# Optimization experiments

Measured on AMD Instinct MI355X. Metric: run time of the kernel, lower is better.

## Reference

```python
import jax, jax.numpy as jnp
import numpy as np

N_STREAMS = 4
N_HEADS = 4
D_STATE = 64
EPS_RMS = float(np.finfo(np.float32).eps)


def rms_norm(x, w):
    v = jnp.mean(x * x, axis=-1, keepdims=True)
    return x * jax.lax.rsqrt(v + EPS_RMS) * w


def sinkhorn_mix(logits, iters=5):
    n = logits.shape[0]
    M = jax.nn.sigmoid(logits) + jnp.eye(n, dtype=logits.dtype)
    for _ in range(iters):
        M = M / (M.sum(axis=1, keepdims=True) + 1e-6)
        M = M / (M.sum(axis=0, keepdims=True) + 1e-6)
    return M


def mamba_block(u, norm_w, Wi, bi, A_log, D, dt_bias, Wo, bo):
    B, L, d_model = u.shape
    d_in = 2 * d_model
    P = d_in // N_HEADS
    un = rms_norm(u, norm_w)
    zxbcdt = un @ Wi + bi  # [B,L,4612]
    z = zxbcdt[:, :, :d_in]
    x = zxbcdt[:, :, d_in:2 * d_in].reshape(B, L, N_HEADS, P)
    dt = zxbcdt[:, :, 2 * d_in:2 * d_in + N_HEADS]
    BC = zxbcdt[:, :, 2 * d_in + N_HEADS:].reshape(B, L, N_HEADS, 2, D_STATE)
    B_mat, C_mat = BC[:, :, :, 0], BC[:, :, :, 1]
    dt = jax.nn.softplus(dt + dt_bias)            # [B,L,H]
    A = -jnp.exp(A_log)                            # [H]
    dtA = jnp.exp(dt * A)                          # [B,L,H]
    dtB = dt[..., None] * B_mat                    # [B,L,H,N]

    # time-major scan over the selective-state recurrence
    def step(h, inp):
        dtA_t, dtB_t, x_t, C_t = inp               # [B,H],[B,H,N],[B,H,P],[B,H,N]
        h = h * dtA_t[:, :, None, None] + dtB_t[..., None] * x_t[:, :, None, :]
        y_t = jnp.einsum('bhn,bhnp->bhp', C_t, h)
        return h, y_t

    h0 = jnp.zeros((B, N_HEADS, D_STATE, P), dtype=u.dtype)
    xs = (jnp.moveaxis(dtA, 1, 0), jnp.moveaxis(dtB, 1, 0),
          jnp.moveaxis(x, 1, 0), jnp.moveaxis(C_mat, 1, 0))
    _, ys = jax.lax.scan(step, h0, xs)             # ys: [L,B,H,P]
    y = jnp.moveaxis(ys, 0, 1)                     # [B,L,H,P]
    y = y + x * D[None, None, :, None]
    y = y.reshape(B, L, d_in) * jax.nn.silu(z)
    return y @ Wo + bo


def setup_inputs() -> dict:
    key = jax.random.key(0)
    ks = jax.random.split(key, 10)
    B, L, d_model, vocab, n_layers = 2, 2048, 1024, 32000, 4
    d_proj_out = 2 * 2 * d_model + 2 * N_HEADS * D_STATE + N_HEADS  # 4612
    d_in = 2 * d_model
    s = lambda f: 1.0 / np.sqrt(f)
    return {
        'tokens': jax.random.randint(ks[0], (B, L), 0, vocab, dtype=jnp.int32),
        'embed': jax.random.normal(ks[1], (vocab, d_model), jnp.float32) * 0.02,
        'norm_w': jnp.ones((n_layers, d_model), jnp.float32),
        'in_proj_W': jax.random.normal(ks[2], (n_layers, d_model, d_proj_out), jnp.float32) * s(d_model),
        'in_proj_b': jnp.zeros((n_layers, d_proj_out), jnp.float32),
        'A_log': jnp.full((n_layers, N_HEADS), -4.0, jnp.float32),
        'D': jnp.ones((n_layers, N_HEADS), jnp.float32),
        'dt_bias': jax.random.uniform(ks[3], (n_layers, N_HEADS), jnp.float32) - 4.0,
        'out_proj_W': jax.random.normal(ks[4], (n_layers, d_in, d_model), jnp.float32) * s(d_in),
        'out_proj_b': jnp.zeros((n_layers, d_model), jnp.float32),
        'mixer_logits': jax.random.normal(ks[5], (n_layers, N_STREAMS, N_STREAMS), jnp.float32) * 0.1,
        'norm_f_w': jnp.ones((d_model,), jnp.float32),
        'head_W': jax.random.normal(ks[6], (d_model, vocab), jnp.float32) * s(d_model),
        'head_b': jnp.zeros((vocab,), jnp.float32),
    }


def reference(tokens, embed, norm_w, in_proj_W, in_proj_b, A_log, D, dt_bias,
              out_proj_W, out_proj_b, mixer_logits, norm_f_w, head_W, head_b):
    B, L = tokens.shape
    d_model = embed.shape[1]
    d_sub = d_model // N_STREAMS
    x = embed[tokens]                              # [B,L,d_model]
    H = x.reshape(B, L, N_STREAMS, d_sub)
    n_layers = norm_w.shape[0]
    for l in range(n_layers):
        M = sinkhorn_mix(mixer_logits[l])
        H_res = jnp.einsum('bsid,ji->bsjd', H, M)
        x_out = mamba_block(H.reshape(B, L, d_model), norm_w[l], in_proj_W[l],
                            in_proj_b[l], A_log[l], D[l], dt_bias[l],
                            out_proj_W[l], out_proj_b[l])
        H = H_res + x_out.reshape(B, L, N_STREAMS, d_sub)
    out = rms_norm(H.reshape(B, L, d_model), norm_f_w)
    return out @ head_W + head_b
```

## Files before the change

kernel.cpp:

```cpp
#include <hip/hip_runtime.h>
#include <hip/hip_fp16.h>
#include <cstdint>


typedef _Float16 f16;
typedef __attribute__((ext_vector_type(8))) _Float16 f16x8;
typedef __attribute__((ext_vector_type(4))) _Float16 f16x4;
typedef __attribute__((ext_vector_type(4))) float f32x4;

#define LDS_CAST(p) ((__attribute__((address_space(3))) void*)(p))
#define GLB_CAST(p) ((const __attribute__((address_space(1))) void*)(p))

static __device__ __forceinline__ void gload16(const void* g, void* l) {
    __builtin_amdgcn_global_load_lds(GLB_CAST(g), LDS_CAST(l), 16, 0, 0);
}

__global__ __launch_bounds__(256) void gemm_f16(
    const f16* __restrict__ A, const f16* __restrict__ Bt,
    const float* __restrict__ bias, float* __restrict__ C,
    int M, int N, int K)
{
    __shared__ f16 As[128 * 32];
    __shared__ f16 Bs[128 * 32];
    const int t = threadIdx.x;
    const int lane = t & 63;
    const int w = t >> 6;
    const int m0 = blockIdx.y * 128, n0 = blockIdx.x * 128;
    const int wm0 = (w >> 1) * 64, wn0 = (w & 1) * 64;
    const int mrow = lane & 15, ksel = lane >> 4;

    f32x4 zero = {0.f, 0.f, 0.f, 0.f};
    f32x4 acc[4][4];
#pragma unroll
    for (int i = 0; i < 4; i++)
#pragma unroll
        for (int j = 0; j < 4; j++) acc[i][j] = zero;

    const f16* Abase = A + (size_t)m0 * K;
    const f16* Bbase = Bt + (size_t)n0 * K;

    for (int k0 = 0; k0 < K; k0 += 32) {
#pragma unroll
        for (int i = 0; i < 2; i++) {
            int lin = t + i * 256;
            int r = lin >> 2;
            int cc = (lin & 3) * 8;
            gload16(Abase + (size_t)r * K + k0 + cc, As + lin * 8);
            gload16(Bbase + (size_t)r * K + k0 + cc, Bs + lin * 8);
        }
        __syncthreads();
        f16x8 af[4], bf[4];
#pragma unroll
        for (int i = 0; i < 4; i++) {
            af[i] = *(const f16x8*)(As + (wm0 + i * 16 + mrow) * 32 + ksel * 8);
            bf[i] = *(const f16x8*)(Bs + (wn0 + i * 16 + mrow) * 32 + ksel * 8);
        }
#pragma unroll
        for (int i = 0; i < 4; i++)
#pragma unroll
            for (int j = 0; j < 4; j++)
                acc[i][j] = __builtin_amdgcn_mfma_f32_16x16x32_f16(af[i], bf[j], acc[i][j], 0, 0, 0);
        __syncthreads();
    }

    const int r0 = ksel * 4;
#pragma unroll
    for (int j = 0; j < 4; j++) {
        int col = n0 + wn0 + j * 16 + mrow;
        if (col < N) {
            float bv = bias ? bias[col] : 0.f;
#pragma unroll
            for (int i = 0; i < 4; i++) {
                int rowm = m0 + wm0 + i * 16 + r0;
#pragma unroll
                for (int r = 0; r < 4; r++)
                    C[(size_t)(rowm + r) * N + col] = acc[i][j][r] + bv;
            }
        }
    }
}

__global__ __launch_bounds__(256) void transpose_w(
    const float* __restrict__ W, f16* __restrict__ Wt, int K, int N, int Npad)
{
    __shared__ float tile[32][33];
    int n0 = blockIdx.x * 32, k0 = blockIdx.y * 32;
    int tx = threadIdx.x & 31, ty = threadIdx.x >> 5;
#pragma unroll
    for (int i = 0; i < 4; i++) {
        int k = k0 + ty + 8 * i;
        int n = n0 + tx;
        tile[ty + 8 * i][tx] = (n < N) ? W[(size_t)k * N + n] : 0.f;
    }
    __syncthreads();
#pragma unroll
    for (int i = 0; i < 4; i++) {
        int n = n0 + ty + 8 * i;
        if (n < Npad) Wt[(size_t)n * K + k0 + tx] = (f16)tile[tx][ty + 8 * i];
    }
}

__global__ void sinkhorn_k(const float* __restrict__ logits, float* __restrict__ Mout)
{
    if (threadIdx.x != 0 || blockIdx.x != 0) return;
    for (int l = 0; l < 4; l++) {
        float M[16];
        for (int i = 0; i < 16; i++) {
            float v = logits[l * 16 + i];
            M[i] = 1.f / (1.f + __expf(-v)) + ((i % 5) == 0 ? 1.f : 0.f);
        }
        for (int it = 0; it < 5; it++) {
            for (int r = 0; r < 4; r++) {
                float s = M[r*4] + M[r*4+1] + M[r*4+2] + M[r*4+3] + 1e-6f;
                for (int c = 0; c < 4; c++) M[r*4+c] /= s;
            }
            for (int c = 0; c < 4; c++) {
                float s = M[c] + M[4+c] + M[8+c] + M[12+c] + 1e-6f;
                for (int r = 0; r < 4; r++) M[r*4+c] /= s;
            }
        }
        for (int i = 0; i < 16; i++) Mout[l * 16 + i] = M[i];
    }
}

__global__ __launch_bounds__(256) void embed_gather(
    const int* __restrict__ tokens, const float* __restrict__ embed, float* __restrict__ H)
{
    int i = blockIdx.x * 256 + threadIdx.x;
    int tok = i >> 8, d4 = i & 255;
    int tk = tokens[tok];
    float4 v = ((const float4*)(embed + (size_t)tk * 1024))[d4];
    ((float4*)(H + (size_t)tok * 1024))[d4] = v;
}

__global__ __launch_bounds__(256) void rmsnorm_k(
    const float* __restrict__ X, const float* __restrict__ w, f16* __restrict__ out)
{
    int tok = blockIdx.x;
    int t = threadIdx.x;
    const float4 v = ((const float4*)(X + (size_t)tok * 1024))[t];
    float ss = v.x*v.x + v.y*v.y + v.z*v.z + v.w*v.w;
#pragma unroll
    for (int off = 32; off > 0; off >>= 1) ss += __shfl_down(ss, off, 64);
    __shared__ float wsum[4];
    if ((t & 63) == 0) wsum[t >> 6] = ss;
    __syncthreads();
    float tot = wsum[0] + wsum[1] + wsum[2] + wsum[3];
    float sc = rsqrtf(tot * (1.f / 1024.f) + 1.1920929e-07f);
    const float4 wv = ((const float4*)w)[t];
    f16x4 o;
    o[0] = (f16)(v.x * sc * wv.x);
    o[1] = (f16)(v.y * sc * wv.y);
    o[2] = (f16)(v.z * sc * wv.z);
    o[3] = (f16)(v.w * sc * wv.w);
    ((f16x4*)(out + (size_t)tok * 1024))[t] = o;
}

__global__ __launch_bounds__(256) void dt_cumsum(
    const float* __restrict__ zx, const float* __restrict__ dt_bias,
    const float* __restrict__ A_log,
    float* __restrict__ dt, float* __restrict__ cum, float* __restrict__ E)
{
    int bh = blockIdx.x;
    int b = bh >> 2, h = bh & 3;
    int t = threadIdx.x;
    float Ah = -__expf(A_log[h]);
    float bias = dt_bias[h];
    float run = 0.f, vals[8];
    for (int i = 0; i < 8; i++) {
        int l = t * 8 + i;
        float raw = zx[((size_t)(b * 2048 + l)) * 4612 + 4096 + h] + bias;
        float dtv = (raw > 20.f) ? raw : log1pf(__expf(raw));
        dt[bh * 2048 + l] = dtv;
        run += dtv * Ah;
        vals[i] = run;
    }
    __shared__ float ps[256];
    ps[t] = run;
    __syncthreads();
    for (int off = 1; off < 256; off <<= 1) {
        float v = (t >= off) ? ps[t - off] : 0.f;
        __syncthreads();
        ps[t] += v;
        __syncthreads();
    }
    float offset = (t > 0) ? ps[t - 1] : 0.f;
    for (int i = 0; i < 8; i++) {
        int l = t * 8 + i;
        float cv = vals[i] + offset;
        cum[bh * 2048 + l] = cv;
        if ((l & 63) == 63) E[bh * 32 + (l >> 6)] = cv;
    }
}

__global__ __launch_bounds__(256) void make_xT(
    const float* __restrict__ zx, f16* __restrict__ xT)
{
    int lb = blockIdx.x * 64, pb = blockIdx.y * 64, bh = blockIdx.z;
    int b = bh >> 2, h = bh & 3;
    __shared__ float tile[64][65];
    int tx = threadIdx.x & 63, ty = threadIdx.x >> 6;
#pragma unroll
    for (int i = 0; i < 16; i++) {
        int ll = ty + 4 * i;
        tile[ll][tx] = zx[((size_t)(b * 2048 + lb + ll)) * 4612 + 2048 + h * 512 + pb + tx];
    }
    __syncthreads();
#pragma unroll
    for (int i = 0; i < 16; i++) {
        int pl = ty + 4 * i;
        xT[((size_t)bh * 512 + pb + pl) * 2048 + lb + tx] = (f16)tile[tx][pl];
    }
}

__global__ __launch_bounds__(256) void make_BC(
    const float* __restrict__ zx, f16* __restrict__ Bc, f16* __restrict__ Cc)
{
    int i = blockIdx.x * 256 + threadIdx.x;
    int n = i & 63, h = (i >> 6) & 3, l = (i >> 8) & 2047, b = i >> 19;
    size_t rowoff = ((size_t)(b * 2048 + l)) * 4612 + 4100 + h * 128;
    size_t o = (((size_t)(b * 4 + h)) * 2048 + l) * 64 + n;
    Bc[o] = (f16)zx[rowoff + n];
    Cc[o] = (f16)zx[rowoff + 64 + n];
}

__global__ __launch_bounds__(256) void chunk_intra(
    const f16* __restrict__ Bc, const f16* __restrict__ Cc,
    const f16* __restrict__ xT,
    const float* __restrict__ dt, const float* __restrict__ cum,
    float* __restrict__ Y, float* __restrict__ Hloc)
{
    int c = blockIdx.x, bh = blockIdx.y;
    int l0 = c * 64;
    __shared__ f16 Cs[4096], Bs2[4096], Sb[4096], Wb[4096];
    __shared__ float cums[64], dts[64];
    int t = threadIdx.x;
    {
        const f16x8* sC = (const f16x8*)(Cc + ((size_t)bh * 2048 + l0) * 64);
        const f16x8* sB = (const f16x8*)(Bc + ((size_t)bh * 2048 + l0) * 64);
        ((f16x8*)Cs)[t] = sC[t];
        ((f16x8*)Cs)[t + 256] = sC[t + 256];
        ((f16x8*)Bs2)[t] = sB[t];
        ((f16x8*)Bs2)[t + 256] = sB[t + 256];
    }
    if (t < 64) {
        cums[t] = cum[bh * 2048 + l0 + t];
        dts[t] = dt[bh * 2048 + l0 + t];
    }
    __syncthreads();
    float cumEnd = cums[63];
#pragma unroll
    for (int q = 0; q < 16; q++) {
        int idx = t * 16 + q;
        int tt = idx >> 6, ss = idx & 63;
        float dot = 0.f;
        for (int n = 0; n < 64; n++)
            dot += (float)Cs[tt * 64 + n] * (float)Bs2[ss * 64 + n];
        float sv = (ss <= tt) ? dot * __expf(cums[tt] - cums[ss]) * dts[ss] : 0.f;
        Sb[idx] = (f16)sv;
        float wv = (float)Bs2[ss * 64 + tt] * __expf(cumEnd - cums[ss]) * dts[ss];
        Wb[tt * 64 + ss] = (f16)wv;
    }
    __syncthreads();

    int lane = t & 63, w = t >> 6;
    int mrow = lane & 15, ksel = lane >> 4;
    f16x8 sfr[2][4], wfr[2][4];
#pragma unroll
    for (int ks = 0; ks < 2; ks++)
#pragma unroll
        for (int mt = 0; mt < 4; mt++) {
            sfr[ks][mt] = *(const f16x8*)(Sb + (mt * 16 + mrow) * 64 + ks * 32 + ksel * 8);
            wfr[ks][mt] = *(const f16x8*)(Wb + (mt * 16 + mrow) * 64 + ks * 32 + ksel * 8);
        }
    const f16* xbase = xT + ((size_t)bh * 512) * 2048 + c * 64;
    f32x4 zero = {0.f, 0.f, 0.f, 0.f};
#pragma unroll
    for (int ph = 0; ph < 2; ph++) {
        int pb = w * 128 + ph * 64;
        f32x4 aY[4][4], aH[4][4];
#pragma unroll
        for (int i = 0; i < 4; i++)
#pragma unroll
            for (int j = 0; j < 4; j++) { aY[i][j] = zero; aH[i][j] = zero; }
#pragma unroll
        for (int ks = 0; ks < 2; ks++) {
#pragma unroll
            for (int nt = 0; nt < 4; nt++) {
                int pp = pb + nt * 16 + mrow;
                f16x8 bfv = *(const f16x8*)(xbase + (size_t)pp * 2048 + ks * 32 + ksel * 8);
#pragma unroll
                for (int mt = 0; mt < 4; mt++) {
                    aY[mt][nt] = __builtin_amdgcn_mfma_f32_16x16x32_f16(sfr[ks][mt], bfv, aY[mt][nt], 0, 0, 0);
                    aH[mt][nt] = __builtin_amdgcn_mfma_f32_16x16x32_f16(wfr[ks][mt], bfv, aH[mt][nt], 0, 0, 0);
                }
            }
        }
        int r0 = ksel * 4;
#pragma unroll
        for (int mt = 0; mt < 4; mt++)
#pragma unroll
            for (int nt = 0; nt < 4; nt++) {
                int pp = pb + nt * 16 + mrow;
#pragma unroll
                for (int r = 0; r < 4; r++) {
                    int tt = mt * 16 + r0 + r;
                    Y[((size_t)bh * 2048 + l0 + tt) * 512 + pp] = aY[mt][nt][r];
                    Hloc[(((size_t)bh * 32 + c) * 64 + tt) * 512 + pp] = aH[mt][nt][r];
                }
            }
    }
}

__global__ __launch_bounds__(256) void chunk_scan(
    const float* __restrict__ Hloc, const float* __restrict__ E,
    f16* __restrict__ HpreT)
{
    int bh = blockIdx.y;
    int p = blockIdx.x * 64 + (threadIdx.x & 63);
    int nb = (threadIdx.x >> 6) * 16;
    float h[16];
#pragma unroll
    for (int j = 0; j < 16; j++) h[j] = 0.f;
    float Eprev = 0.f;
    for (int c = 0; c < 32; c++) {
        size_t ob = (((size_t)bh * 32 + c) * 512 + p) * 64 + nb;
        f16x8 v0, v1;
#pragma unroll
        for (int j = 0; j < 8; j++) { v0[j] = (f16)h[j]; v1[j] = (f16)h[j + 8]; }
        *(f16x8*)(HpreT + ob) = v0;
        *(f16x8*)(HpreT + ob + 8) = v1;
        float Ec = E[bh * 32 + c];
        float decay = __expf(Ec - Eprev);
        Eprev = Ec;
        size_t ib = (((size_t)bh * 32 + c) * 64 + nb) * 512 + p;
#pragma unroll
        for (int j = 0; j < 16; j++)
            h[j] = decay * h[j] + Hloc[ib + (size_t)j * 512];
    }
}

__global__ __launch_bounds__(256) void chunk_inter(
    const f16* __restrict__ Cc, const f16* __restrict__ HpreT,
    const float* __restrict__ cum, const float* __restrict__ E,
    const float* __restrict__ Y, const float* __restrict__ zx,
    const float* __restrict__ Dp, f16* __restrict__ ybuf)
{
    int c = blockIdx.x, bh = blockIdx.y;
    int b = bh >> 2, h = bh & 3;
    int l0 = c * 64;
    __shared__ f16 Chat[4096];
    int t = threadIdx.x;
    float Eprev = (c > 0) ? E[bh * 32 + c - 1] : 0.f;
    for (int i = t; i < 4096; i += 256) {
        int tt = i >> 6, n = i & 63;
        float cv = (float)Cc[((size_t)bh * 2048 + l0 + tt) * 64 + n];
        Chat[i] = (f16)(cv * __expf(cum[bh * 2048 + l0 + tt] - Eprev));
    }
    __syncthreads();
    int lane = t & 63, w = t >> 6;
    int mrow = lane & 15, ksel = lane >> 4;
    float Dh = Dp[h];
    f16x8 af[2][4];
#pragma unroll
    for (int ks = 0; ks < 2; ks++)
#pragma unroll
        for (int mt = 0; mt < 4; mt++)
            af[ks][mt] = *(const f16x8*)(Chat + (mt * 16 + mrow) * 64 + ks * 32 + ksel * 8);
    const f16* hb = HpreT + (((size_t)bh * 32 + c) * 512) * 64;
    f32x4 zero = {0.f, 0.f, 0.f, 0.f};
#pragma unroll
    for (int ph = 0; ph < 2; ph++) {
        int pb = w * 128 + ph * 64;
        f32x4 acc[4][4];
#pragma unroll
        for (int i = 0; i < 4; i++)
#pragma unroll
            for (int j = 0; j < 4; j++) acc[i][j] = zero;
#pragma unroll
        for (int ks = 0; ks < 2; ks++) {
#pragma unroll
            for (int nt = 0; nt < 4; nt++) {
                int pp = pb + nt * 16 + mrow;
                f16x8 bfv = *(const f16x8*)(hb + (size_t)pp * 64 + ks * 32 + ksel * 8);
#pragma unroll
                for (int mt = 0; mt < 4; mt++)
                    acc[mt][nt] = __builtin_amdgcn_mfma_f32_16x16x32_f16(af[ks][mt], bfv, acc[mt][nt], 0, 0, 0);
            }
        }
        int r0 = ksel * 4;
#pragma unroll
        for (int mt = 0; mt < 4; mt++)
#pragma unroll
            for (int nt = 0; nt < 4; nt++) {
                int pp = pb + nt * 16 + mrow;
#pragma unroll
                for (int r = 0; r < 4; r++) {
                    int tt = mt * 16 + r0 + r;
                    int l = l0 + tt;
                    size_t zrow = ((size_t)(b * 2048 + l)) * 4612;
                    float y = acc[mt][nt][r] + Y[((size_t)bh * 2048 + l) * 512 + pp];
                    float x = zx[zrow + 2048 + h * 512 + pp];
                    y += x * Dh;
                    float z = zx[zrow + h * 512 + pp];
                    float sig = 1.f / (1.f + __expf(-z));
                    ybuf[((size_t)(b * 2048 + l)) * 2048 + h * 512 + pp] = (f16)(y * z * sig);
                }
            }
    }
}

__global__ __launch_bounds__(256) void mix_add(
    const float* __restrict__ Hold, const float* __restrict__ xout,
    const float* __restrict__ Mm, float* __restrict__ Hnew)
{
    int i = blockIdx.x * 256 + threadIdx.x;
    int j = i & 255, tok = i >> 8;
    size_t rb = (size_t)tok * 1024;
    float h0 = Hold[rb + j], h1 = Hold[rb + 256 + j];
    float h2 = Hold[rb + 512 + j], h3 = Hold[rb + 768 + j];
#pragma unroll
    for (int s = 0; s < 4; s++) {
        float v = Mm[s*4+0]*h0 + Mm[s*4+1]*h1 + Mm[s*4+2]*h2 + Mm[s*4+3]*h3
                + xout[rb + s * 256 + j];
        Hnew[rb + s * 256 + j] = v;
    }
}

extern "C" void kernel_launch(void* const* d_in, const int* in_sizes, int n_in,
                              void* d_out, int out_size, void* d_ws, size_t ws_size,
                              hipStream_t stream)
{
    const int*   tokens     = (const int*)d_in[0];
    const float* embed      = (const float*)d_in[1];
    const float* norm_w     = (const float*)d_in[2];
    const float* in_proj_W  = (const float*)d_in[3];
    const float* in_proj_b  = (const float*)d_in[4];
    const float* A_log      = (const float*)d_in[5];
    const float* Dp         = (const float*)d_in[6];
    const float* dt_bias    = (const float*)d_in[7];
    const float* out_proj_W = (const float*)d_in[8];
    const float* out_proj_b = (const float*)d_in[9];
    const float* mixer_log  = (const float*)d_in[10];
    const float* norm_f_w   = (const float*)d_in[11];
    const float* head_W     = (const float*)d_in[12];
    const float* head_b     = (const float*)d_in[13];
    float* out = (float*)d_out;
    (void)in_sizes; (void)n_in; (void)out_size; (void)ws_size;

    char* base = (char*)d_ws;
    size_t off = 0;
    auto alloc = [&](size_t bytes) -> void* {
        void* r = (void*)(base + off);
        off = (off + bytes + 255) & ~(size_t)255;
        return r;
    };
    f16*   WinT   = (f16*)alloc(4ull * 4736 * 1024 * 2);
    f16*   WoutT  = (f16*)alloc(4ull * 1024 * 2048 * 2);
    f16*   WheadT = (f16*)alloc(32000ull * 1024 * 2);
    float* Mall   = (float*)alloc(64 * 4);
    float* H0     = (float*)alloc(4096ull * 1024 * 4);
    float* H1     = (float*)alloc(4096ull * 1024 * 4);
    f16*   un     = (f16*)alloc(4096ull * 1024 * 2);
    float* zx     = (float*)alloc(4096ull * 4612 * 4);
    float* dtb    = (float*)alloc(8ull * 2048 * 4);
    float* cumb   = (float*)alloc(8ull * 2048 * 4);
    float* Eb     = (float*)alloc(8ull * 32 * 4);
    f16*   xT     = (f16*)alloc(8ull * 512 * 2048 * 2);
    f16*   Bc     = (f16*)alloc(8ull * 2048 * 64 * 2);
    f16*   Cc     = (f16*)alloc(8ull * 2048 * 64 * 2);
    float* Yb     = (float*)alloc(8ull * 2048 * 512 * 4);
    float* Hloc   = (float*)alloc(8ull * 32 * 64 * 512 * 4);
    f16*   HpreT  = (f16*)alloc(8ull * 32 * 512 * 64 * 2);
    f16*   ybuf   = (f16*)alloc(4096ull * 2048 * 2);
    float* xout   = (float*)alloc(4096ull * 1024 * 4);

    for (int l = 0; l < 4; l++) {
        transpose_w<<<dim3(148, 32), 256, 0, stream>>>(
            in_proj_W + (size_t)l * 1024 * 4612, WinT + (size_t)l * 4736 * 1024,
            1024, 4612, 4736);
        transpose_w<<<dim3(32, 64), 256, 0, stream>>>(
            out_proj_W + (size_t)l * 2048 * 1024, WoutT + (size_t)l * 1024 * 2048,
            2048, 1024, 1024);
    }
    transpose_w<<<dim3(1000, 32), 256, 0, stream>>>(head_W, WheadT, 1024, 32000, 32000);
    sinkhorn_k<<<1, 64, 0, stream>>>(mixer_log, Mall);
    embed_gather<<<4096, 256, 0, stream>>>(tokens, embed, H0);

    float* Hc = H0;
    float* Hn = H1;
    for (int l = 0; l < 4; l++) {
        rmsnorm_k<<<4096, 256, 0, stream>>>(Hc, norm_w + l * 1024, un);
        gemm_f16<<<dim3(37, 32), 256, 0, stream>>>(
            un, WinT + (size_t)l * 4736 * 1024, in_proj_b + l * 4612, zx,
            4096, 4612, 1024);
        dt_cumsum<<<8, 256, 0, stream>>>(zx, dt_bias + l * 4, A_log + l * 4, dtb, cumb, Eb);
        make_xT<<<dim3(32, 8, 8), 256, 0, stream>>>(zx, xT);
        make_BC<<<4096, 256, 0, stream>>>(zx, Bc, Cc);
        chunk_intra<<<dim3(32, 8), 256, 0, stream>>>(Bc, Cc, xT, dtb, cumb, Yb, Hloc);
        chunk_scan<<<dim3(8, 8), 256, 0, stream>>>(Hloc, Eb, HpreT);
        chunk_inter<<<dim3(32, 8), 256, 0, stream>>>(Cc, HpreT, cumb, Eb, Yb, zx, Dp + l * 4, ybuf);
        gemm_f16<<<dim3(8, 32), 256, 0, stream>>>(
            ybuf, WoutT + (size_t)l * 1024 * 2048, out_proj_b + l * 1024, xout,
            4096, 1024, 2048);
        mix_add<<<4096, 256, 0, stream>>>(Hc, xout, Mall + l * 16, Hn);
        float* tmp = Hc; Hc = Hn; Hn = tmp;
    }
    rmsnorm_k<<<4096, 256, 0, stream>>>(Hc, norm_f_w, un);
    gemm_f16<<<dim3(250, 32), 256, 0, stream>>>(un, WheadT, head_b, out, 4096, 32000, 1024);
}
```

Baseline: 2.273 ms.

## Swizzle GEMM tile order for XCD locality, vectorize epilogue, MFMA intra-chunk scores

The GEMM now remaps block IDs so consecutive work-groups on each XCD cover grouped M tiles. This improves L2 reuse of the weight and activation panels, and the grid dimensions are swapped to match. The MFMA operands are swapped so each lane holds four consecutive N columns, which allows float4 stores and bias loads in place of scalar strided stores. The chunk_intra C·B score computation moves from scalar per-thread dot products to MFMA. chunk_scan is split across a third grid dimension for more parallelism. The swizzle mapping treats the grid's x as the M-tile count, which relies on the launch dims being set consistently. The float4 accesses assume N is a multiple of four.

```diff
diff --git a/kernel.cpp b/kernel.cpp
--- a/kernel.cpp
+++ b/kernel.cpp
@@ -25,7 +25,24 @@
     const int t = threadIdx.x;
     const int lane = t & 63;
     const int w = t >> 6;
-    const int m0 = blockIdx.y * 128, n0 = blockIdx.x * 128;
+
+    const int gx = gridDim.x;
+    const int gy = gridDim.y;
+    const int nwg = gx * gy;
+    int lin = blockIdx.y * gx + blockIdx.x;
+    int xcd = lin & 7, loc = lin >> 3;
+    int q = nwg >> 3, rr = nwg & 7;
+    int wg = (xcd < rr) ? (xcd * (q + 1) + loc)
+                        : (rr * (q + 1) + (xcd - rr) * q + loc);
+    const int GROUP = 8;
+    int per_group = GROUP * gy;
+    int gid = wg / per_group;
+    int first_m = gid * GROUP;
+    int gsz = (gx - first_m < GROUP) ? (gx - first_m) : GROUP;
+    int inner = wg - gid * per_group;
+    const int m0 = (first_m + inner % gsz) * 128;
+    const int n0 = (inner / gsz) * 128;
+
     const int wm0 = (w >> 1) * 64, wn0 = (w & 1) * 64;
     const int mrow = lane & 15, ksel = lane >> 4;
 
@@ -42,11 +59,11 @@
     for (int k0 = 0; k0 < K; k0 += 32) {
 #pragma unroll
         for (int i = 0; i < 2; i++) {
-            int lin = t + i * 256;
-            int r = lin >> 2;
-            int cc = (lin & 3) * 8;
-            gload16(Abase + (size_t)r * K + k0 + cc, As + lin * 8);
-            gload16(Bbase + (size_t)r * K + k0 + cc, Bs + lin * 8);
+            int lin2 = t + i * 256;
+            int r = lin2 >> 2;
+            int cc = (lin2 & 3) * 8;
+            gload16(Abase + (size_t)r * K + k0 + cc, As + lin2 * 8);
+            gload16(Bbase + (size_t)r * K + k0 + cc, Bs + lin2 * 8);
         }
         __syncthreads();
         f16x8 af[4], bf[4];
@@ -59,22 +76,25 @@
         for (int i = 0; i < 4; i++)
 #pragma unroll
             for (int j = 0; j < 4; j++)
-                acc[i][j] = __builtin_amdgcn_mfma_f32_16x16x32_f16(af[i], bf[j], acc[i][j], 0, 0, 0);
+                acc[i][j] = __builtin_amdgcn_mfma_f32_16x16x32_f16(bf[j], af[i], acc[i][j], 0, 0, 0);
         __syncthreads();
     }
 
-    const int r0 = ksel * 4;
-#pragma unroll
-    for (int j = 0; j < 4; j++) {
-        int col = n0 + wn0 + j * 16 + mrow;
-        if (col < N) {
-            float bv = bias ? bias[col] : 0.f;
-#pragma unroll
-            for (int i = 0; i < 4; i++) {
-                int rowm = m0 + wm0 + i * 16 + r0;
-#pragma unroll
-                for (int r = 0; r < 4; r++)
-                    C[(size_t)(rowm + r) * N + col] = acc[i][j][r] + bv;
+#pragma unroll
+    for (int i = 0; i < 4; i++) {
+        int m = m0 + wm0 + i * 16 + mrow;
+#pragma unroll
+        for (int j = 0; j < 4; j++) {
+            int nb = n0 + wn0 + j * 16 + ksel * 4;
+            if (nb < N) {
+                float4 bv = {0.f, 0.f, 0.f, 0.f};
+                if (bias) bv = *(const float4*)(bias + nb);
+                float4 v;
+                v.x = acc[i][j][0] + bv.x;
+                v.y = acc[i][j][1] + bv.y;
+                v.z = acc[i][j][2] + bv.z;
+                v.w = acc[i][j][3] + bv.w;
+                *(float4*)(C + (size_t)m * N + nb) = v;
             }
         }
     }
@@ -249,22 +269,39 @@
     }
     __syncthreads();
     float cumEnd = cums[63];
-#pragma unroll
-    for (int q = 0; q < 16; q++) {
-        int idx = t * 16 + q;
-        int tt = idx >> 6, ss = idx & 63;
-        float dot = 0.f;
-        for (int n = 0; n < 64; n++)
-            dot += (float)Cs[tt * 64 + n] * (float)Bs2[ss * 64 + n];
-        float sv = (ss <= tt) ? dot * __expf(cums[tt] - cums[ss]) * dts[ss] : 0.f;
-        Sb[idx] = (f16)sv;
-        float wv = (float)Bs2[ss * 64 + tt] * __expf(cumEnd - cums[ss]) * dts[ss];
-        Wb[tt * 64 + ss] = (f16)wv;
-    }
-    __syncthreads();
-
     int lane = t & 63, w = t >> 6;
     int mrow = lane & 15, ksel = lane >> 4;
+
+    {
+        f16x8 cf[2];
+        cf[0] = *(const f16x8*)(Cs + (w * 16 + mrow) * 64 + ksel * 8);
+        cf[1] = *(const f16x8*)(Cs + (w * 16 + mrow) * 64 + 32 + ksel * 8);
+#pragma unroll
+        for (int j = 0; j < 4; j++) {
+            f32x4 d = {0.f, 0.f, 0.f, 0.f};
+#pragma unroll
+            for (int ks = 0; ks < 2; ks++) {
+                f16x8 bfv = *(const f16x8*)(Bs2 + (j * 16 + mrow) * 64 + ks * 32 + ksel * 8);
+                d = __builtin_amdgcn_mfma_f32_16x16x32_f16(cf[ks], bfv, d, 0, 0, 0);
+            }
+            int ss = j * 16 + mrow;
+#pragma unroll
+            for (int r = 0; r < 4; r++) {
+                int tt = w * 16 + ksel * 4 + r;
+                float sv = (ss <= tt) ? d[r] * __expf(cums[tt] - cums[ss]) * dts[ss] : 0.f;
+                Sb[tt * 64 + ss] = (f16)sv;
+            }
+        }
+#pragma unroll
+        for (int q2 = 0; q2 < 16; q2++) {
+            int idx = t * 16 + q2;
+            int tt = idx >> 6, ss = idx & 63;
+            float wv = (float)Bs2[ss * 64 + tt] * __expf(cumEnd - cums[ss]) * dts[ss];
+            Wb[tt * 64 + ss] = (f16)wv;
+        }
+    }
+    __syncthreads();
+
     f16x8 sfr[2][4], wfr[2][4];
 #pragma unroll
     for (int ks = 0; ks < 2; ks++)
@@ -318,24 +355,23 @@
 {
     int bh = blockIdx.y;
     int p = blockIdx.x * 64 + (threadIdx.x & 63);
-    int nb = (threadIdx.x >> 6) * 16;
-    float h[16];
-#pragma unroll
-    for (int j = 0; j < 16; j++) h[j] = 0.f;
+    int nb = blockIdx.z * 16 + (threadIdx.x >> 6) * 4;
+    float h[4];
+#pragma unroll
+    for (int j = 0; j < 4; j++) h[j] = 0.f;
     float Eprev = 0.f;
     for (int c = 0; c < 32; c++) {
         size_t ob = (((size_t)bh * 32 + c) * 512 + p) * 64 + nb;
-        f16x8 v0, v1;
-#pragma unroll
-        for (int j = 0; j < 8; j++) { v0[j] = (f16)h[j]; v1[j] = (f16)h[j + 8]; }
-        *(f16x8*)(HpreT + ob) = v0;
-        *(f16x8*)(HpreT + ob + 8) = v1;
+        f16x4 v;
+#pragma unroll
+        for (int j = 0; j < 4; j++) v[j] = (f16)h[j];
+        *(f16x4*)(HpreT + ob) = v;
         float Ec = E[bh * 32 + c];
         float decay = __expf(Ec - Eprev);
         Eprev = Ec;
         size_t ib = (((size_t)bh * 32 + c) * 64 + nb) * 512 + p;
 #pragma unroll
-        for (int j = 0; j < 16; j++)
+        for (int j = 0; j < 4; j++)
             h[j] = decay * h[j] + Hloc[ib + (size_t)j * 512];
     }
 }
@@ -491,21 +527,21 @@
     float* Hn = H1;
     for (int l = 0; l < 4; l++) {
         rmsnorm_k<<<4096, 256, 0, stream>>>(Hc, norm_w + l * 1024, un);
-        gemm_f16<<<dim3(37, 32), 256, 0, stream>>>(
+        gemm_f16<<<dim3(32, 37), 256, 0, stream>>>(
             un, WinT + (size_t)l * 4736 * 1024, in_proj_b + l * 4612, zx,
             4096, 4612, 1024);
         dt_cumsum<<<8, 256, 0, stream>>>(zx, dt_bias + l * 4, A_log + l * 4, dtb, cumb, Eb);
         make_xT<<<dim3(32, 8, 8), 256, 0, stream>>>(zx, xT);
         make_BC<<<4096, 256, 0, stream>>>(zx, Bc, Cc);
         chunk_intra<<<dim3(32, 8), 256, 0, stream>>>(Bc, Cc, xT, dtb, cumb, Yb, Hloc);
-        chunk_scan<<<dim3(8, 8), 256, 0, stream>>>(Hloc, Eb, HpreT);
+        chunk_scan<<<dim3(8, 8, 4), 256, 0, stream>>>(Hloc, Eb, HpreT);
         chunk_inter<<<dim3(32, 8), 256, 0, stream>>>(Cc, HpreT, cumb, Eb, Yb, zx, Dp + l * 4, ybuf);
-        gemm_f16<<<dim3(8, 32), 256, 0, stream>>>(
+        gemm_f16<<<dim3(32, 8), 256, 0, stream>>>(
             ybuf, WoutT + (size_t)l * 1024 * 2048, out_proj_b + l * 1024, xout,
             4096, 1024, 2048);
         mix_add<<<4096, 256, 0, stream>>>(Hc, xout, Mall + l * 16, Hn);
         float* tmp = Hc; Hc = Hn; Hn = tmp;
     }
     rmsnorm_k<<<4096, 256, 0, stream>>>(Hc, norm_f_w, un);
-    gemm_f16<<<dim3(250, 32), 256, 0, stream>>>(un, WheadT, head_b, out, 4096, 32000, 1024);
-}
+    gemm_f16<<<dim3(32, 250), 256, 0, stream>>>(un, WheadT, head_b, out, 4096, 32000, 1024);
+}
```

Result: faster. 2.130 ms (-6.3%).
